# Kernel optimization log

Hardware: AMD Instinct MI355X
Metric: run time of the kernel (lower is better)

The kernel has to match this reference:

```python
import jax, jax.numpy as jnp
import numpy as np

V, B, L, NG = 50000, 128, 350, 3        # vocab, batch(docs), doc length, n-gram window
D, H, C = 768, 256, 20                  # bert dim, num_hidden, class_num
HEADS, LAYERS, K, ALPHA = 8, 2, 3, 0.15 # GAT heads/layers, diffusion hops k, alpha


def setup_inputs() -> dict:
    rng = np.random.default_rng(0)
    # per-doc graphs: 350 unique word-ids per doc (nodes), n-gram window edges
    node_ids = np.stack([rng.choice(V, L, replace=False) for _ in range(B)]).ravel()
    src_b, dst_b = [], []
    for i in range(L):
        for j in range(max(0, i - NG), min(L, i + NG + 1)):
            src_b.append(i); dst_b.append(j)
    src_b, dst_b = np.asarray(src_b), np.asarray(dst_b)
    off = (np.arange(B) * L)[:, None]
    edge_src = (src_b[None, :] + off).ravel()
    edge_dst = (dst_b[None, :] + off).ravel()
    graph_id = np.repeat(np.arange(B), L)

    ks = jax.random.split(jax.random.key(0), 8)
    f32 = jnp.float32
    return {
        'node_ids': jnp.asarray(node_ids, jnp.int32),
        'edge_src': jnp.asarray(edge_src, jnp.int32),
        'edge_dst': jnp.asarray(edge_dst, jnp.int32),
        'graph_id': jnp.asarray(graph_id, jnp.int32),
        'emb':    (jax.random.normal(ks[0], (V, D), f32) * 0.02),
        'W1':     (jax.random.normal(ks[1], (D, H), f32) / np.sqrt(D)).astype(f32),
        'b1':     jnp.zeros((H,), f32),
        'W2':     (jax.random.normal(ks[2], (H, C), f32) / np.sqrt(H)).astype(f32),
        'b2':     jnp.zeros((C,), f32),
        'gat_W':  (jax.random.normal(ks[3], (LAYERS, HEADS, C, C), f32) / np.sqrt(C)).astype(f32),
        'a_src':  (jax.random.normal(ks[4], (LAYERS, HEADS, C), f32) * 0.1),
        'a_dst':  (jax.random.normal(ks[5], (LAYERS, HEADS, C), f32) * 0.1),
        'w_gate': (jax.random.normal(ks[6], (C,), f32) / np.sqrt(C)).astype(f32),
        'b_gate': jnp.zeros((), f32),
    }


def _gat_layer(h, W, a_s, a_d, src, dst, N):
    # h: [N,C]; W: [Hd,C,C]; a_s/a_d: [Hd,C]
    z = jnp.einsum('nc,hcd->hnd', h, W)                     # [Hd,N,C]
    e = jax.nn.leaky_relu(jnp.einsum('hnd,hd->hn', z, a_s)[:, src]
                          + jnp.einsum('hnd,hd->hn', z, a_d)[:, dst], 0.2)  # [Hd,E]

    def segsoftmax(ev):  # edge softmax over incoming edges at each dst node
        m = jax.ops.segment_max(ev, dst, num_segments=N)
        ex = jnp.exp(ev - m[dst])
        s = jax.ops.segment_sum(ex, dst, num_segments=N)
        return ex / (s[dst] + 1e-9)

    att = jax.vmap(segsoftmax)(e)                           # [Hd,E]

    def diffuse(zh, ah):  # attention diffusion: Z_t = (1-a) A Z_{t-1} + a Z_0
        zt = zh
        for _ in range(K):
            agg = jax.ops.segment_sum(ah[:, None] * zt[src], dst, num_segments=N)
            zt = (1.0 - ALPHA) * agg + ALPHA * zh
        return zt

    out = jax.vmap(diffuse)(z, att)                         # [Hd,N,C]
    return jax.nn.elu(out).mean(axis=0)                     # merge='mean'


def reference(node_ids, edge_src, edge_dst, graph_id, emb, W1, b1, W2, b2,
              gat_W, a_src, a_dst, w_gate, b_gate):
    N = node_ids.shape[0]
    x = emb[node_ids]                                       # [N,768] gather
    x = jax.nn.relu(x @ W1 + b1)                            # linear1 + ReLU
    h = x @ W2 + b2                                         # linear2 -> [N,C]
    for l in range(LAYERS):
        h = _gat_layer(h, gat_W[l], a_src[l], a_dst[l], edge_src, edge_dst, N)
    gate = jax.nn.sigmoid(h @ w_gate + b_gate)[:, None]     # WeightAndSum gate
    return jax.ops.segment_sum(gate * h, graph_id, num_segments=B)  # [B,C]
```

## Files before the change

### kernel.cpp

```cpp
#include <hip/hip_runtime.h>
#include <hip/hip_bf16.h>
#include <cstddef>

#define NB_NODES 44800
#define NDOCS 128
#define DLEN 350
#define DIM 768
#define HID 256
#define NCLS 20
#define NHEADS 8
#define ZSTR 20

typedef __bf16 v8bf __attribute__((ext_vector_type(8)));
typedef float v4f __attribute__((ext_vector_type(4)));

__global__ __launch_bounds__(256) void k_transpose(const float* __restrict__ W1,
                                                   __bf16* __restrict__ W1T) {
  __shared__ float tile[32][33];
  int bx = blockIdx.x % 24;
  int by = blockIdx.x / 24;
  int tx = threadIdx.x & 31, ty = threadIdx.x >> 5;
  int k0 = bx * 32, n0 = by * 32;
#pragma unroll
  for (int i = 0; i < 4; ++i)
    tile[ty + i * 8][tx] = W1[(size_t)(k0 + ty + i * 8) * 256 + n0 + tx];
  __syncthreads();
#pragma unroll
  for (int i = 0; i < 4; ++i)
    W1T[(size_t)(n0 + ty + i * 8) * 768 + k0 + tx] = (__bf16)tile[tx][ty + i * 8];
}

__global__ __launch_bounds__(256) void k_mlp(
    const int* __restrict__ node_ids, const float* __restrict__ emb,
    const __bf16* __restrict__ W1T, const float* __restrict__ b1,
    const float* __restrict__ W2, const float* __restrict__ b2,
    float* __restrict__ h0) {
  __shared__ __align__(16) char smem[33024];
  __bf16* As = (__bf16*)smem;
  float*  xs = (float*)smem;
  int tid = threadIdx.x;
  int wave = tid >> 6, lane = tid & 63;
  int quad = lane >> 4, l16 = lane & 15;
  int m0 = blockIdx.x * 64;

  int lrow = tid & 15;
  int lk4  = (tid >> 4) & 3;
  int khalf = (tid >> 6) & 1;
  int msubA = tid >> 7;
  int kbase = khalf * 32 + lk4 * 8;
  const float* apA = emb + (size_t)node_ids[m0 + msubA * 16 + lrow] * DIM + kbase;
  const float* apB = emb + (size_t)node_ids[m0 + (msubA + 2) * 16 + lrow] * DIM + kbase;

  v4f acc[4][4];
#pragma unroll
  for (int ms = 0; ms < 4; ++ms)
#pragma unroll
    for (int j = 0; j < 4; ++j) acc[ms][j] = (v4f){0.f, 0.f, 0.f, 0.f};

  v4f pf[4];
  pf[0] = *(const v4f*)(apA); pf[1] = *(const v4f*)(apA + 4);
  pf[2] = *(const v4f*)(apB); pf[3] = *(const v4f*)(apB + 4);

  for (int kc = 0; kc < 12; ++kc) {
    __bf16* buf = As + (kc & 1) * 4096;
    v8bf w0, w1;
#pragma unroll
    for (int e = 0; e < 4; ++e) {
      w0[e] = (__bf16)pf[0][e]; w0[4 + e] = (__bf16)pf[1][e];
      w1[e] = (__bf16)pf[2][e]; w1[4 + e] = (__bf16)pf[3][e];
    }
    *(v8bf*)(buf + tid * 8) = w0;
    *(v8bf*)(buf + tid * 8 + 2048) = w1;
    if (kc < 11) {
      int k1 = (kc + 1) * 64;
      pf[0] = *(const v4f*)(apA + k1); pf[1] = *(const v4f*)(apA + k1 + 4);
      pf[2] = *(const v4f*)(apB + k1); pf[3] = *(const v4f*)(apB + k1 + 4);
    }
    __syncthreads();

    v8bf bv[2][4];
#pragma unroll
    for (int ks = 0; ks < 2; ++ks)
#pragma unroll
      for (int j = 0; j < 4; ++j)
        bv[ks][j] = *(const v8bf*)(W1T + (size_t)(wave * 64 + j * 16 + l16) * DIM + kc * 64 + ks * 32 + quad * 8);
#pragma unroll
    for (int ks = 0; ks < 2; ++ks) {
      v8bf af[4];
#pragma unroll
      for (int ms = 0; ms < 4; ++ms)
        af[ms] = *(const v8bf*)(buf + ((ms * 2 + ks) * 64 + lane) * 8);
#pragma unroll
      for (int ms = 0; ms < 4; ++ms)
#pragma unroll
        for (int j = 0; j < 4; ++j)
          acc[ms][j] = __builtin_amdgcn_mfma_f32_16x16x32_bf16(af[ms], bv[ks][j], acc[ms][j], 0, 0, 0);
    }
  }

  __syncthreads();

#pragma unroll
  for (int p = 0; p < 2; ++p) {
    if (p) __syncthreads();
#pragma unroll
    for (int mh = 0; mh < 2; ++mh) {
      int ms = p * 2 + mh;
#pragma unroll
      for (int j = 0; j < 4; ++j) {
        int col = wave * 64 + j * 16 + l16;
        float bb = b1[col];
#pragma unroll
        for (int r = 0; r < 4; ++r) {
          int lr = mh * 16 + quad * 4 + r;
          float v = acc[ms][j][r] + bb;
          xs[lr * 258 + col] = v > 0.f ? v : 0.f;
        }
      }
    }
    __syncthreads();
    if (tid < 160) {
      int m = tid / 5, c0 = (tid % 5) * 4;
      v4f s = *(const v4f*)(b2 + c0);
      for (int k = 0; k < HID; ++k) {
        float x = xs[m * 258 + k];
        v4f w = *(const v4f*)(W2 + k * NCLS + c0);
        s[0] += x * w[0]; s[1] += x * w[1];
        s[2] += x * w[2]; s[3] += x * w[3];
      }
      *(v4f*)(h0 + (size_t)(m0 + p * 32 + m) * NCLS + c0) = s;
    }
  }
}

__global__ __launch_bounds__(384) void k_gat(
    const float* __restrict__ hin, const float* __restrict__ gatW,
    const float* __restrict__ a_src, const float* __restrict__ a_dst,
    int layer, float* __restrict__ zout) {
  __shared__ float zA[DLEN * ZSTR];
  __shared__ float asv[DLEN], adv[DLEN];
  int tid = threadIdx.x;
  int head = blockIdx.x & 7;
  int doc = blockIdx.x >> 3;
  const float* W  = gatW  + (size_t)(layer * NHEADS + head) * NCLS * NCLS;
  const float* av = a_src + (layer * NHEADS + head) * NCLS;
  const float* dv = a_dst + (layer * NHEADS + head) * NCLS;
  int r = tid;
  bool act = r < DLEN;

  float z0[NCLS];
  if (act) {
    const float* hr = hin + ((size_t)doc * DLEN + r) * NCLS;
    float h[NCLS];
#pragma unroll
    for (int q = 0; q < 5; ++q) {
      v4f t = *(const v4f*)(hr + q * 4);
#pragma unroll
      for (int e = 0; e < 4; ++e) h[q * 4 + e] = t[e];
    }
    float zacc[NCLS];
#pragma unroll
    for (int d = 0; d < NCLS; ++d) zacc[d] = 0.f;
#pragma unroll
    for (int c = 0; c < NCLS; ++c) {
      float hc = h[c];
#pragma unroll
      for (int d = 0; d < NCLS; ++d) zacc[d] += hc * W[c * NCLS + d];
    }
    float sa = 0.f, sd = 0.f;
#pragma unroll
    for (int d = 0; d < NCLS; ++d) { sa += zacc[d] * av[d]; sd += zacc[d] * dv[d]; }
    asv[r] = sa; adv[r] = sd;
#pragma unroll
    for (int q = 0; q < 5; ++q) {
      v4f t;
#pragma unroll
      for (int e = 0; e < 4; ++e) t[e] = zacc[q * 4 + e];
      *(v4f*)(zA + r * ZSTR + q * 4) = t;
    }
#pragma unroll
    for (int d = 0; d < NCLS; ++d) z0[d] = zacc[d];
  }
  __syncthreads();

  float att[7];
  if (act) {
    float ad = adv[r];
    float e[7]; float m = -1e30f;
#pragma unroll
    for (int j = 0; j < 7; ++j) {
      int s = r - 3 + j;
      bool valid = (s >= 0) && (s < DLEN);
      float x = valid ? asv[s] + ad : -1e30f;
      x = x > 0.f ? x : 0.2f * x;
      e[j] = valid ? x : -1e30f;
      if (e[j] > m) m = e[j];
    }
    float sum = 0.f;
#pragma unroll
    for (int j = 0; j < 7; ++j) {
      float ex = (e[j] > -1e29f) ? expf(e[j] - m) : 0.f;
      e[j] = ex; sum += ex;
    }
    float inv = 1.f / (sum + 1e-9f);
#pragma unroll
    for (int j = 0; j < 7; ++j) att[j] = e[j] * inv;
  }

  float vn[NCLS];
  for (int hop = 0; hop < 3; ++hop) {
    if (act) {
      v4f agg[5];
#pragma unroll
      for (int q = 0; q < 5; ++q) agg[q] = (v4f){0.f, 0.f, 0.f, 0.f};
#pragma unroll
      for (int j = 0; j < 7; ++j) {
        int s = r - 3 + j;
        s = s < 0 ? 0 : (s > DLEN - 1 ? DLEN - 1 : s);
        float a = att[j];
#pragma unroll
        for (int q = 0; q < 5; ++q) {
          v4f zq = *(const v4f*)(zA + s * ZSTR + q * 4);
#pragma unroll
          for (int e = 0; e < 4; ++e) agg[q][e] += a * zq[e];
        }
      }
#pragma unroll
      for (int q = 0; q < 5; ++q)
#pragma unroll
        for (int e = 0; e < 4; ++e)
          vn[q * 4 + e] = 0.85f * agg[q][e] + 0.15f * z0[q * 4 + e];
    }
    if (hop < 2) {
      __syncthreads();
      if (act) {
#pragma unroll
        for (int q = 0; q < 5; ++q) {
          v4f t;
#pragma unroll
          for (int e = 0; e < 4; ++e) t[e] = vn[q * 4 + e];
          *(v4f*)(zA + r * ZSTR + q * 4) = t;
        }
      }
      __syncthreads();
    }
  }

  if (act) {
    float* og = zout + ((size_t)head * NB_NODES + (size_t)doc * DLEN + r) * NCLS;
#pragma unroll
    for (int q = 0; q < 5; ++q) {
      v4f t;
#pragma unroll
      for (int e = 0; e < 4; ++e) {
        float x = vn[q * 4 + e];
        t[e] = x > 0.f ? x : expf(x) - 1.f;
      }
      *(v4f*)(og + q * 4) = t;
    }
  }
}

__global__ __launch_bounds__(256) void k_headmean(
    const float* __restrict__ eluzt, float* __restrict__ hout) {
  int idx = blockIdx.x * 256 + threadIdx.x;
  v4f s = (v4f){0.f, 0.f, 0.f, 0.f};
#pragma unroll
  for (int h = 0; h < NHEADS; ++h)
    s += ((const v4f*)eluzt)[(size_t)h * (NB_NODES * NCLS / 4) + idx];
  v4f o; o[0] = s[0] * 0.125f; o[1] = s[1] * 0.125f; o[2] = s[2] * 0.125f; o[3] = s[3] * 0.125f;
  ((v4f*)hout)[idx] = o;
}

__global__ __launch_bounds__(64) void k_pool(
    const float* __restrict__ hfin, const float* __restrict__ w_gate,
    const float* __restrict__ b_gate, float* __restrict__ out) {
  int b = blockIdx.x, lane = threadIdx.x;
  float wg[NCLS];
#pragma unroll
  for (int c = 0; c < NCLS; ++c) wg[c] = w_gate[c];
  float bg = b_gate[0];
  float acc[NCLS];
#pragma unroll
  for (int c = 0; c < NCLS; ++c) acc[c] = 0.f;
  for (int n = lane; n < DLEN; n += 64) {
    const v4f* hr = (const v4f*)(hfin + ((size_t)b * DLEN + n) * NCLS);
    float hv[NCLS];
    float d = bg;
#pragma unroll
    for (int q = 0; q < 5; ++q) {
      v4f t = hr[q];
#pragma unroll
      for (int j = 0; j < 4; ++j) { hv[q * 4 + j] = t[j]; d += t[j] * wg[q * 4 + j]; }
    }
    float g = 1.f / (1.f + expf(-d));
#pragma unroll
    for (int c = 0; c < NCLS; ++c) acc[c] += g * hv[c];
  }
#pragma unroll
  for (int off = 32; off > 0; off >>= 1)
#pragma unroll
    for (int c = 0; c < NCLS; ++c) acc[c] += __shfl_down(acc[c], off);
  if (lane == 0)
#pragma unroll
    for (int c = 0; c < NCLS; ++c) out[b * NCLS + c] = acc[c];
}

extern "C" void kernel_launch(void* const* d_in, const int* in_sizes, int n_in,
                              void* d_out, int out_size, void* d_ws, size_t ws_size,
                              hipStream_t stream) {
  const int* node_ids = (const int*)d_in[0];
  const float* emb    = (const float*)d_in[4];
  const float* W1     = (const float*)d_in[5];
  const float* b1     = (const float*)d_in[6];
  const float* W2     = (const float*)d_in[7];
  const float* b2     = (const float*)d_in[8];
  const float* gatW   = (const float*)d_in[9];
  const float* a_src  = (const float*)d_in[10];
  const float* a_dst  = (const float*)d_in[11];
  const float* w_gate = (const float*)d_in[12];
  const float* b_gate = (const float*)d_in[13];
  float* out = (float*)d_out;
  char* ws = (char*)d_ws;

  __bf16* W1T = (__bf16*)(ws + 0);
  float* hA  = (float*)(ws + 393216);
  float* hB  = (float*)(ws + 3977216);
  float* zt  = (float*)(ws + 7561216);

  k_transpose<<<192, 256, 0, stream>>>(W1, W1T);
  k_mlp<<<NB_NODES / 64, 256, 0, stream>>>(node_ids, emb, W1T, b1, W2, b2, hA);
  k_gat<<<NDOCS * NHEADS, 384, 0, stream>>>(hA, gatW, a_src, a_dst, 0, zt);
  k_headmean<<<(NB_NODES * NCLS / 4) / 256, 256, 0, stream>>>(zt, hB);
  k_gat<<<NDOCS * NHEADS, 384, 0, stream>>>(hB, gatW, a_src, a_dst, 1, zt);
  k_headmean<<<(NB_NODES * NCLS / 4) / 256, 256, 0, stream>>>(zt, hA);
  k_pool<<<NDOCS, 64, 0, stream>>>(hA, w_gate, b_gate, out);
}
```

Measured before the change: 368.1 us.

## Split embedding gather into bf16 staging kernel and load MFMA operands directly

Adds a separate gather kernel that converts the gathered fp32 embedding rows to a bf16 matrix in workspace. The MLP kernel then loads A and B fragments straight from global memory into registers with double-buffered prefetch, removing the LDS staging and per-chunk barriers. The pooling kernel grows from one wave to four waves per document and combines the partial sums through shared memory. The cost is an extra launch and an extra write and read of a 44800x768 bf16 buffer, which shares workspace with zt (safe because zt is written later).

```diff
diff --git a/kernel.cpp b/kernel.cpp
--- a/kernel.cpp
+++ b/kernel.cpp
@@ -12,6 +12,7 @@
 #define ZSTR 20
 
 typedef __bf16 v8bf __attribute__((ext_vector_type(8)));
+typedef __bf16 v4bf __attribute__((ext_vector_type(4)));
 typedef float v4f __attribute__((ext_vector_type(4)));
 
 __global__ __launch_bounds__(256) void k_transpose(const float* __restrict__ W1,
@@ -30,26 +31,37 @@
     W1T[(size_t)(n0 + ty + i * 8) * 768 + k0 + tx] = (__bf16)tile[tx][ty + i * 8];
 }
 
+__global__ __launch_bounds__(256) void k_gather(const int* __restrict__ node_ids,
+                                                const float* __restrict__ emb,
+                                                __bf16* __restrict__ Ab) {
+  int idx = blockIdx.x * 256 + threadIdx.x;
+  int row = idx / 192, off = (idx - row * 192) * 4;
+  const float* src = emb + (size_t)node_ids[row] * DIM + off;
+  v4f v = *(const v4f*)src;
+  v4bf o;
+#pragma unroll
+  for (int e = 0; e < 4; ++e) o[e] = (__bf16)v[e];
+  *(v4bf*)(Ab + (size_t)row * DIM + off) = o;
+}
+
 __global__ __launch_bounds__(256) void k_mlp(
-    const int* __restrict__ node_ids, const float* __restrict__ emb,
-    const __bf16* __restrict__ W1T, const float* __restrict__ b1,
-    const float* __restrict__ W2, const float* __restrict__ b2,
-    float* __restrict__ h0) {
-  __shared__ __align__(16) char smem[33024];
-  __bf16* As = (__bf16*)smem;
-  float*  xs = (float*)smem;
+    const __bf16* __restrict__ Ab, const __bf16* __restrict__ W1T,
+    const float* __restrict__ b1, const float* __restrict__ W2,
+    const float* __restrict__ b2, float* __restrict__ h0) {
+  __shared__ float xs[32 * 260];
   int tid = threadIdx.x;
   int wave = tid >> 6, lane = tid & 63;
   int quad = lane >> 4, l16 = lane & 15;
   int m0 = blockIdx.x * 64;
 
-  int lrow = tid & 15;
-  int lk4  = (tid >> 4) & 3;
-  int khalf = (tid >> 6) & 1;
-  int msubA = tid >> 7;
-  int kbase = khalf * 32 + lk4 * 8;
-  const float* apA = emb + (size_t)node_ids[m0 + msubA * 16 + lrow] * DIM + kbase;
-  const float* apB = emb + (size_t)node_ids[m0 + (msubA + 2) * 16 + lrow] * DIM + kbase;
+  const __bf16* Arow[4];
+#pragma unroll
+  for (int ms = 0; ms < 4; ++ms)
+    Arow[ms] = Ab + (size_t)(m0 + ms * 16 + l16) * DIM + quad * 8;
+  const __bf16* Brow[4];
+#pragma unroll
+  for (int j = 0; j < 4; ++j)
+    Brow[j] = W1T + (size_t)(wave * 64 + j * 16 + l16) * DIM + quad * 8;
 
   v4f acc[4][4];
 #pragma unroll
@@ -57,48 +69,37 @@
 #pragma unroll
     for (int j = 0; j < 4; ++j) acc[ms][j] = (v4f){0.f, 0.f, 0.f, 0.f};
 
-  v4f pf[4];
-  pf[0] = *(const v4f*)(apA); pf[1] = *(const v4f*)(apA + 4);
-  pf[2] = *(const v4f*)(apB); pf[3] = *(const v4f*)(apB + 4);
-
-  for (int kc = 0; kc < 12; ++kc) {
-    __bf16* buf = As + (kc & 1) * 4096;
-    v8bf w0, w1;
-#pragma unroll
-    for (int e = 0; e < 4; ++e) {
-      w0[e] = (__bf16)pf[0][e]; w0[4 + e] = (__bf16)pf[1][e];
-      w1[e] = (__bf16)pf[2][e]; w1[4 + e] = (__bf16)pf[3][e];
-    }
-    *(v8bf*)(buf + tid * 8) = w0;
-    *(v8bf*)(buf + tid * 8 + 2048) = w1;
-    if (kc < 11) {
-      int k1 = (kc + 1) * 64;
-      pf[0] = *(const v4f*)(apA + k1); pf[1] = *(const v4f*)(apA + k1 + 4);
-      pf[2] = *(const v4f*)(apB + k1); pf[3] = *(const v4f*)(apB + k1 + 4);
-    }
-    __syncthreads();
-
-    v8bf bv[2][4];
+  v8bf a0[8], b0[8], a1[8], b1r[8];
+  auto LD = [&](int kc, v8bf* a, v8bf* b) {
+#pragma unroll
+    for (int ms = 0; ms < 4; ++ms)
+#pragma unroll
+      for (int ks = 0; ks < 2; ++ks)
+        a[ms * 2 + ks] = *(const v8bf*)(Arow[ms] + kc * 64 + ks * 32);
+#pragma unroll
+    for (int j = 0; j < 4; ++j)
+#pragma unroll
+      for (int ks = 0; ks < 2; ++ks)
+        b[j * 2 + ks] = *(const v8bf*)(Brow[j] + kc * 64 + ks * 32);
+  };
+  auto FMA = [&](v8bf* a, v8bf* b) {
 #pragma unroll
     for (int ks = 0; ks < 2; ++ks)
 #pragma unroll
-      for (int j = 0; j < 4; ++j)
-        bv[ks][j] = *(const v8bf*)(W1T + (size_t)(wave * 64 + j * 16 + l16) * DIM + kc * 64 + ks * 32 + quad * 8);
-#pragma unroll
-    for (int ks = 0; ks < 2; ++ks) {
-      v8bf af[4];
-#pragma unroll
       for (int ms = 0; ms < 4; ++ms)
-        af[ms] = *(const v8bf*)(buf + ((ms * 2 + ks) * 64 + lane) * 8);
-#pragma unroll
-      for (int ms = 0; ms < 4; ++ms)
 #pragma unroll
         for (int j = 0; j < 4; ++j)
-          acc[ms][j] = __builtin_amdgcn_mfma_f32_16x16x32_bf16(af[ms], bv[ks][j], acc[ms][j], 0, 0, 0);
-    }
-  }
-
-  __syncthreads();
+          acc[ms][j] = __builtin_amdgcn_mfma_f32_16x16x32_bf16(
+              a[ms * 2 + ks], b[j * 2 + ks], acc[ms][j], 0, 0, 0);
+  };
+
+  LD(0, a0, b0);
+  for (int kc = 0; kc < 12; kc += 2) {
+    if (kc + 1 < 12) LD(kc + 1, a1, b1r);
+    FMA(a0, b0);
+    if (kc + 2 < 12) LD(kc + 2, a0, b0);
+    FMA(a1, b1r);
+  }
 
 #pragma unroll
   for (int p = 0; p < 2; ++p) {
@@ -114,7 +115,7 @@
         for (int r = 0; r < 4; ++r) {
           int lr = mh * 16 + quad * 4 + r;
           float v = acc[ms][j][r] + bb;
-          xs[lr * 258 + col] = v > 0.f ? v : 0.f;
+          xs[lr * 260 + col] = v > 0.f ? v : 0.f;
         }
       }
     }
@@ -123,7 +124,7 @@
       int m = tid / 5, c0 = (tid % 5) * 4;
       v4f s = *(const v4f*)(b2 + c0);
       for (int k = 0; k < HID; ++k) {
-        float x = xs[m * 258 + k];
+        float x = xs[m * 260 + k];
         v4f w = *(const v4f*)(W2 + k * NCLS + c0);
         s[0] += x * w[0]; s[1] += x * w[1];
         s[2] += x * w[2]; s[3] += x * w[3];
@@ -272,10 +273,12 @@
   ((v4f*)hout)[idx] = o;
 }
 
-__global__ __launch_bounds__(64) void k_pool(
+__global__ __launch_bounds__(256) void k_pool(
     const float* __restrict__ hfin, const float* __restrict__ w_gate,
     const float* __restrict__ b_gate, float* __restrict__ out) {
-  int b = blockIdx.x, lane = threadIdx.x;
+  __shared__ float red[4][NCLS];
+  int b = blockIdx.x, tid = threadIdx.x;
+  int wave = tid >> 6, lane = tid & 63;
   float wg[NCLS];
 #pragma unroll
   for (int c = 0; c < NCLS; ++c) wg[c] = w_gate[c];
@@ -283,7 +286,7 @@
   float acc[NCLS];
 #pragma unroll
   for (int c = 0; c < NCLS; ++c) acc[c] = 0.f;
-  for (int n = lane; n < DLEN; n += 64) {
+  for (int n = tid; n < DLEN; n += 256) {
     const v4f* hr = (const v4f*)(hfin + ((size_t)b * DLEN + n) * NCLS);
     float hv[NCLS];
     float d = bg;
@@ -303,7 +306,10 @@
     for (int c = 0; c < NCLS; ++c) acc[c] += __shfl_down(acc[c], off);
   if (lane == 0)
 #pragma unroll
-    for (int c = 0; c < NCLS; ++c) out[b * NCLS + c] = acc[c];
+    for (int c = 0; c < NCLS; ++c) red[wave][c] = acc[c];
+  __syncthreads();
+  if (tid < NCLS)
+    out[b * NCLS + tid] = red[0][tid] + red[1][tid] + red[2][tid] + red[3][tid];
 }
 
 extern "C" void kernel_launch(void* const* d_in, const int* in_sizes, int n_in,
@@ -326,13 +332,15 @@
   __bf16* W1T = (__bf16*)(ws + 0);
   float* hA  = (float*)(ws + 393216);
   float* hB  = (float*)(ws + 3977216);
+  __bf16* Ab = (__bf16*)(ws + 7561216);
   float* zt  = (float*)(ws + 7561216);
 
   k_transpose<<<192, 256, 0, stream>>>(W1, W1T);
-  k_mlp<<<NB_NODES / 64, 256, 0, stream>>>(node_ids, emb, W1T, b1, W2, b2, hA);
+  k_gather<<<NB_NODES * 192 / 256, 256, 0, stream>>>(node_ids, emb, Ab);
+  k_mlp<<<NB_NODES / 64, 256, 0, stream>>>(Ab, W1T, b1, W2, b2, hA);
   k_gat<<<NDOCS * NHEADS, 384, 0, stream>>>(hA, gatW, a_src, a_dst, 0, zt);
   k_headmean<<<(NB_NODES * NCLS / 4) / 256, 256, 0, stream>>>(zt, hB);
   k_gat<<<NDOCS * NHEADS, 384, 0, stream>>>(hB, gatW, a_src, a_dst, 1, zt);
   k_headmean<<<(NB_NODES * NCLS / 4) / 256, 256, 0, stream>>>(zt, hA);
-  k_pool<<<NDOCS, 64, 0, stream>>>(hA, w_gate, b_gate, out);
-}
+  k_pool<<<NDOCS, 256, 0, stream>>>(hA, w_gate, b_gate, out);
+}
```

Result: slower. 417.4 us (+13.4%).
